# Kernel tuning notes

Measured on AMD Instinct MI355X. Metric: run time of the kernel, lower is better.

Reference implementation:

```python
import jax, jax.numpy as jnp
import numpy as np

DIM = 2
WIDTH = 128
N = 262144
T = 101
W0 = 44.0


def setup_inputs() -> dict:
    key = jax.random.key(0)
    ks = jax.random.split(key, 7)
    # time grid: arange scaled to [0, 1] (dt = 0.01)
    t = jnp.arange(T, dtype=jnp.float32) / (T - 1)
    x0 = jax.random.normal(ks[0], (N, DIM), dtype=jnp.float32)
    # SIREN init: first layer U(-1/dim, 1/dim); later layers U(-sqrt(6/fan_in)/w0, +)
    c0 = 1.0 / DIM
    ch = float(np.sqrt(6.0 / WIDTH) / W0)
    W1 = jax.random.uniform(ks[1], (DIM, WIDTH), jnp.float32, -c0, c0)
    b1 = jax.random.uniform(ks[2], (WIDTH,), jnp.float32, -c0, c0)
    W2 = jax.random.uniform(ks[3], (WIDTH, WIDTH), jnp.float32, -ch, ch)
    b2 = jax.random.uniform(ks[4], (WIDTH,), jnp.float32, -ch, ch)
    W3 = jax.random.uniform(ks[5], (WIDTH, DIM), jnp.float32, -ch, ch)
    b3 = jax.random.uniform(ks[6], (DIM,), jnp.float32, -ch, ch)
    return {"t": t, "x0": x0, "W1": W1, "b1": b1, "W2": W2, "b2": b2, "W3": W3, "b3": b3}


def reference(t, x0, W1, b1, W2, b2, W3, b3):
    def f(x):
        h = jnp.sin(W0 * (x @ W1 + b1))   # [N, WIDTH]
        h = jnp.sin(W0 * (h @ W2 + b2))   # [N, WIDTH]
        return h @ W3 + b3                # [N, DIM]

    # torchdiffeq fixed-grid 'rk4' uses the 3/8-rule (rk4_alt_step_func)
    def step(y, dt):
        k1 = f(y)
        k2 = f(y + dt * k1 / 3.0)
        k3 = f(y + dt * (k2 - k1 / 3.0))
        k4 = f(y + dt * (k1 - k2 + k3))
        y1 = y + (k1 + 3.0 * (k2 + k3) + k4) * dt * 0.125
        return y1, y1

    dts = t[1:] - t[:-1]                  # [T-1]
    _, ys = jax.lax.scan(step, x0, dts)   # [T-1, N, DIM]
    return jnp.concatenate([x0[None], ys], axis=0)  # [T, N, DIM]
```

## Files before the change

kernel.cpp:

```cpp
#include <hip/hip_runtime.h>


#define W0F    44.0f
#define INV2PI 0.15915494309189535f
#define SCALE  (W0F * INV2PI)
#define WIDTH  128
#define NPART  262144
#define TSTEPS 101

typedef short s16x8 __attribute__((ext_vector_type(8)));
typedef float f32x4 __attribute__((ext_vector_type(4)));

__device__ __forceinline__ float sin_rev(float z) {
    return __builtin_amdgcn_sinf(__builtin_amdgcn_fractf(z));
}
__device__ __forceinline__ unsigned short f2bf(float x) {
    __bf16 b = (__bf16)x;
    return __builtin_bit_cast(unsigned short, b);
}
__device__ __forceinline__ float bf2f(unsigned short u) {
    unsigned int v = ((unsigned int)u) << 16;
    return __builtin_bit_cast(float, v);
}

#define ROR_ADD(x, ctrl) ((x) + __builtin_bit_cast(float, \
    __builtin_amdgcn_update_dpp(0, __builtin_bit_cast(int, (x)), (ctrl), 0xF, 0xF, false)))
__device__ __forceinline__ float row_sum16(float x) {
    x = ROR_ADD(x, 0x128);
    x = ROR_ADD(x, 0x124);
    x = ROR_ADD(x, 0x122);
    x = ROR_ADD(x, 0x121);
    return x;
}

__device__ __forceinline__ float sel16(const float g[16], int idx) {
    float a[8], b[4], c[2];
    #pragma unroll
    for (int i = 0; i < 8; ++i) a[i] = (idx & 8) ? g[i + 8] : g[i];
    #pragma unroll
    for (int i = 0; i < 4; ++i) b[i] = (idx & 4) ? a[i + 4] : a[i];
    #pragma unroll
    for (int i = 0; i < 2; ++i) c[i] = (idx & 2) ? b[i + 2] : b[i];
    return (idx & 1) ? c[1] : c[0];
}

__global__ void prep_kernel(const float* __restrict__ W1, const float* __restrict__ b1,
                            const float* __restrict__ W2, float* __restrict__ ws) {
    int i = blockIdx.x * blockDim.x + threadIdx.x;
    unsigned short* whi = (unsigned short*)ws;
    unsigned short* wlo = whi + 16384;
    if (i < 16384) {
        int j = i & 7, l = (i >> 3) & 63, c = (i >> 9) & 3, nt = (i >> 11) & 7;
        int k = 32 * c + 8 * (l >> 4) + j;
        int n = 16 * nt + (l & 15);
        float v = SCALE * W2[k * WIDTH + n];
        unsigned short hi = f2bf(v);
        whi[i] = hi;
        wlo[i] = f2bf(v - bf2f(hi));
    }
    if (i < 2 * WIDTH) ws[16384 + i] = SCALE * W1[i];
    if (i < WIDTH)     ws[16384 + 256 + i] = SCALE * b1[i];
}

__launch_bounds__(256, 2)
__global__ void ode_kernel(const float* __restrict__ t,
                           const float2* __restrict__ x0,
                           const float* __restrict__ ws,
                           const float* __restrict__ W3,
                           const float* __restrict__ b2,
                           const float* __restrict__ b3,
                           float2* __restrict__ out) {
    __shared__ unsigned int sBh[8192];
    __shared__ unsigned int sBl[8192];
    __shared__ __align__(16) float sWx[WIDTH], sWy[WIDTH], sWb[WIDTH];
    __shared__ float2 sW3[WIDTH];
    __shared__ float  sB2[WIDTH];

    const int tid = threadIdx.x;
    const int wave = tid >> 6;
    const int lane = tid & 63;
    const int lane15 = lane & 15;
    const int kg = lane >> 4;

    {
        const uint4* srch = (const uint4*)ws;
        const uint4* srcl = (const uint4*)(ws + 8192);
        uint4* dsth = (uint4*)sBh;
        uint4* dstl = (uint4*)sBl;
        #pragma unroll
        for (int j = 0; j < 8; ++j) {
            dsth[tid + 256 * j] = srch[tid + 256 * j];
            dstl[tid + 256 * j] = srcl[tid + 256 * j];
        }
    }
    if (tid < WIDTH) {
        sWx[tid] = ws[16384 + tid];
        sWy[tid] = ws[16384 + WIDTH + tid];
        sWb[tid] = ws[16384 + 256 + tid];
        sW3[tid] = make_float2(W3[2 * tid], W3[2 * tid + 1]);
        sB2[tid] = SCALE * b2[tid];
    }
    __syncthreads();

    const int mloc = 16 * (lane15 >> 2) + 4 * kg + (lane15 & 3);
    const int p = blockIdx.x * 256 + wave * 64 + mloc;

    float2 y = x0[p];
    out[p] = y;

    const float b30 = b3[0], b31 = b3[1];

    float tprev = t[0];
    #pragma unroll 1
    for (int step = 0; step < TSTEPS - 1; ++step) {
        const float tnext = t[step + 1];
        const float dt = tnext - tprev;
        tprev = tnext;

        float k1x=0.f,k1y=0.f,k2x=0.f,k2y=0.f,k3x=0.f,k3y=0.f,sx=0.f,sy=0.f;

        #pragma unroll 1
        for (int s = 0; s < 4; ++s) {
            float yinx, yiny;
            if (s == 0)      { yinx = y.x;                                 yiny = y.y; }
            else if (s == 1) { const float c1 = dt * (1.0f / 3.0f);
                               yinx = y.x + c1 * k1x;                       yiny = y.y + c1 * k1y; }
            else if (s == 2) { yinx = y.x + dt * (k2x - (1.0f/3.0f) * k1x); yiny = y.y + dt * (k2y - (1.0f/3.0f) * k1y); }
            else             { yinx = y.x + dt * (k1x - k2x + k3x);         yiny = y.y + dt * (k1y - k2y + k3y); }

            float qx[4], qy[4];
            {
                const int sbase = 16 * (lane15 >> 2) + (lane15 & 3);
                qx[0] = __shfl(yinx, sbase,      64); qy[0] = __shfl(yiny, sbase,      64);
                qx[1] = __shfl(yinx, sbase + 4,  64); qy[1] = __shfl(yiny, sbase + 4,  64);
                qx[2] = __shfl(yinx, sbase + 8,  64); qy[2] = __shfl(yiny, sbase + 8,  64);
                qx[3] = __shfl(yinx, sbase + 12, 64); qy[3] = __shfl(yiny, sbase + 12, 64);
            }

            f32x4 acc[8][4];
            #pragma unroll
            for (int i = 0; i < 8; ++i) {
                const float bb = sB2[16 * i + lane15];
                const f32x4 v4 = (f32x4){bb, bb, bb, bb};
                #pragma unroll
                for (int mt = 0; mt < 4; ++mt) acc[i][mt] = v4;
            }

            #pragma unroll 1
            for (int c = 0; c < 4; ++c) {
                uint4 ah[4], al[4];
                #pragma unroll
                for (int jq = 0; jq < 2; ++jq) {
                    float4 wxv = *(const float4*)&sWx[32 * c + 8 * kg + 4 * jq];
                    float4 wyv = *(const float4*)&sWy[32 * c + 8 * kg + 4 * jq];
                    float4 wbv = *(const float4*)&sWb[32 * c + 8 * kg + 4 * jq];
                    #pragma unroll
                    for (int mt = 0; mt < 4; ++mt) {
                        float v0 = sin_rev(fmaf(qx[mt], wxv.x, fmaf(qy[mt], wyv.x, wbv.x)));
                        float v1 = sin_rev(fmaf(qx[mt], wxv.y, fmaf(qy[mt], wyv.y, wbv.y)));
                        float v2 = sin_rev(fmaf(qx[mt], wxv.z, fmaf(qy[mt], wyv.z, wbv.z)));
                        float v3 = sin_rev(fmaf(qx[mt], wxv.w, fmaf(qy[mt], wyv.w, wbv.w)));
                        unsigned short h0 = f2bf(v0), h1 = f2bf(v1);
                        unsigned short h2 = f2bf(v2), h3 = f2bf(v3);
                        unsigned int hA = (unsigned int)h0 | ((unsigned int)h1 << 16);
                        unsigned int hB = (unsigned int)h2 | ((unsigned int)h3 << 16);
                        unsigned int lA = (unsigned int)f2bf(v0 - bf2f(h0)) |
                                          ((unsigned int)f2bf(v1 - bf2f(h1)) << 16);
                        unsigned int lB = (unsigned int)f2bf(v2 - bf2f(h2)) |
                                          ((unsigned int)f2bf(v3 - bf2f(h3)) << 16);
                        if (jq == 0) { ah[mt].x = hA; ah[mt].y = hB;
                                       al[mt].x = lA; al[mt].y = lB; }
                        else         { ah[mt].z = hA; ah[mt].w = hB;
                                       al[mt].z = lA; al[mt].w = lB; }
                    }
                }

                #pragma unroll
                for (int nt = 0; nt < 8; ++nt) {
                    const int fo = (nt * 4 + c) * 256 + lane * 4;
                    uint4 bhU = *(const uint4*)&sBh[fo];
                    uint4 blU = *(const uint4*)&sBl[fo];
                    s16x8 bh = __builtin_bit_cast(s16x8, bhU);
                    s16x8 bl = __builtin_bit_cast(s16x8, blU);
                    #pragma unroll
                    for (int mt = 0; mt < 4; ++mt) {
                        s16x8 ahv = __builtin_bit_cast(s16x8, ah[mt]);
                        s16x8 alv = __builtin_bit_cast(s16x8, al[mt]);
                        acc[nt][mt] = __builtin_amdgcn_mfma_f32_16x16x32_bf16(ahv, bh, acc[nt][mt], 0, 0, 0);
                        acc[nt][mt] = __builtin_amdgcn_mfma_f32_16x16x32_bf16(alv, bh, acc[nt][mt], 0, 0, 0);
                        acc[nt][mt] = __builtin_amdgcn_mfma_f32_16x16x32_bf16(ahv, bl, acc[nt][mt], 0, 0, 0);
                    }
                }
            }

            float gx[16], gy[16];
            #pragma unroll
            for (int i = 0; i < 16; ++i) { gx[i] = 0.f; gy[i] = 0.f; }
            #pragma unroll
            for (int nt = 0; nt < 8; ++nt) {
                float2 w3v = sW3[16 * nt + lane15];
                #pragma unroll
                for (int mt = 0; mt < 4; ++mt) {
                    #pragma unroll
                    for (int r = 0; r < 4; ++r) {
                        float sn = sin_rev(acc[nt][mt][r]);
                        gx[4*mt+r] = fmaf(sn, w3v.x, gx[4*mt+r]);
                        gy[4*mt+r] = fmaf(sn, w3v.y, gy[4*mt+r]);
                    }
                }
            }
            #pragma unroll
            for (int i = 0; i < 16; ++i) { gx[i] = row_sum16(gx[i]); gy[i] = row_sum16(gy[i]); }
            const float fx = b30 + sel16(gx, lane15);
            const float fy = b31 + sel16(gy, lane15);

            if (s == 0)      { k1x = fx; k1y = fy; sx = fx;        sy = fy; }
            else if (s == 1) { k2x = fx; k2y = fy; sx += 3.f * fx; sy += 3.f * fy; }
            else if (s == 2) { k3x = fx; k3y = fy; sx += 3.f * fx; sy += 3.f * fy; }
            else             {                     sx += fx;       sy += fy; }
        }

        const float cc = dt * 0.125f;
        y.x += sx * cc;
        y.y += sy * cc;
        out[(size_t)(step + 1) * NPART + p] = y;
    }
}

extern "C" void kernel_launch(void* const* d_in, const int* in_sizes, int n_in,
                              void* d_out, int out_size, void* d_ws, size_t ws_size,
                              hipStream_t stream) {
    const float*  t  = (const float*)d_in[0];
    const float2* x0 = (const float2*)d_in[1];
    const float*  W1 = (const float*)d_in[2];
    const float*  b1 = (const float*)d_in[3];
    const float*  W2 = (const float*)d_in[4];
    const float*  b2 = (const float*)d_in[5];
    const float*  W3 = (const float*)d_in[6];
    const float*  b3 = (const float*)d_in[7];
    float* ws = (float*)d_ws;
    float2* out = (float2*)d_out;

    prep_kernel<<<64, 256, 0, stream>>>(W1, b1, W2, ws);
    ode_kernel<<<NPART / 256, 256, 0, stream>>>(t, x0, ws, W3, b2, b3, out);
}
```

Before: 10.42 ms.

## Software-pipeline layer-1 sin/A-fragment build with MFMA chunks, cheaper bf16 split

The K-chunk loop is fully unrolled with double-buffered A fragments, so the sin evaluation and bf16 packing for the next chunk can overlap with the MFMAs of the current chunk. The hi/lo bf16 split now truncates and packs with v_perm instead of rounding conversions, which cuts VALU work at slightly lower precision in the hi part. The fract range reduction before sin is also dropped, relying on the hardware sin accepting unreduced revolutions. This raises register pressure under the 2-blocks launch bound and may lose accuracy for large arguments.

```diff
diff --git a/kernel.cpp b/kernel.cpp
--- a/kernel.cpp
+++ b/kernel.cpp
@@ -12,7 +12,7 @@
 typedef float f32x4 __attribute__((ext_vector_type(4)));
 
 __device__ __forceinline__ float sin_rev(float z) {
-    return __builtin_amdgcn_sinf(__builtin_amdgcn_fractf(z));
+    return __builtin_amdgcn_sinf(z);
 }
 __device__ __forceinline__ unsigned short f2bf(float x) {
     __bf16 b = (__bf16)x;
@@ -21,6 +21,14 @@
 __device__ __forceinline__ float bf2f(unsigned short u) {
     unsigned int v = ((unsigned int)u) << 16;
     return __builtin_bit_cast(float, v);
+}
+__device__ __forceinline__ float trunc16f(float v) {
+    return __builtin_bit_cast(float, __builtin_bit_cast(unsigned int, v) & 0xffff0000u);
+}
+__device__ __forceinline__ unsigned int pack_hi16(float vlo, float vhi) {
+    return __builtin_amdgcn_perm(__builtin_bit_cast(unsigned int, vhi),
+                                 __builtin_bit_cast(unsigned int, vlo),
+                                 0x07060302u);
 }
 
 #define ROR_ADD(x, ctrl) ((x) + __builtin_bit_cast(float, \
@@ -62,6 +70,34 @@
     if (i < WIDTH)     ws[16384 + 256 + i] = SCALE * b1[i];
 }
 
+#define BUILD_A(cc, AH, AL)                                                          \
+    {                                                                                \
+        _Pragma("unroll")                                                            \
+        for (int jq = 0; jq < 2; ++jq) {                                             \
+            float4 wxv = *(const float4*)&sWx[32 * (cc) + 8 * kg + 4 * jq];          \
+            float4 wyv = *(const float4*)&sWy[32 * (cc) + 8 * kg + 4 * jq];          \
+            float4 wbv = *(const float4*)&sWb[32 * (cc) + 8 * kg + 4 * jq];          \
+            _Pragma("unroll")                                                        \
+            for (int mt = 0; mt < 4; ++mt) {                                         \
+                float v0 = sin_rev(fmaf(qx[mt], wxv.x, fmaf(qy[mt], wyv.x, wbv.x))); \
+                float v1 = sin_rev(fmaf(qx[mt], wxv.y, fmaf(qy[mt], wyv.y, wbv.y))); \
+                float v2 = sin_rev(fmaf(qx[mt], wxv.z, fmaf(qy[mt], wyv.z, wbv.z))); \
+                float v3 = sin_rev(fmaf(qx[mt], wxv.w, fmaf(qy[mt], wyv.w, wbv.w))); \
+                float r0 = v0 - trunc16f(v0);                                        \
+                float r1 = v1 - trunc16f(v1);                                        \
+                float r2 = v2 - trunc16f(v2);                                        \
+                float r3 = v3 - trunc16f(v3);                                        \
+                if (jq == 0) {                                                       \
+                    AH[mt].x = pack_hi16(v0, v1); AH[mt].y = pack_hi16(v2, v3);      \
+                    AL[mt].x = pack_hi16(r0, r1); AL[mt].y = pack_hi16(r2, r3);      \
+                } else {                                                             \
+                    AH[mt].z = pack_hi16(v0, v1); AH[mt].w = pack_hi16(v2, v3);      \
+                    AL[mt].z = pack_hi16(r0, r1); AL[mt].w = pack_hi16(r2, r3);      \
+                }                                                                    \
+            }                                                                        \
+        }                                                                            \
+    }
+
 __launch_bounds__(256, 2)
 __global__ void ode_kernel(const float* __restrict__ t,
                            const float2* __restrict__ x0,
@@ -146,34 +182,11 @@
                 for (int mt = 0; mt < 4; ++mt) acc[i][mt] = v4;
             }
 
-            #pragma unroll 1
+            uint4 ah[2][4], al[2][4];
+            BUILD_A(0, ah[0], al[0])
+            #pragma unroll
             for (int c = 0; c < 4; ++c) {
-                uint4 ah[4], al[4];
-                #pragma unroll
-                for (int jq = 0; jq < 2; ++jq) {
-                    float4 wxv = *(const float4*)&sWx[32 * c + 8 * kg + 4 * jq];
-                    float4 wyv = *(const float4*)&sWy[32 * c + 8 * kg + 4 * jq];
-                    float4 wbv = *(const float4*)&sWb[32 * c + 8 * kg + 4 * jq];
-                    #pragma unroll
-                    for (int mt = 0; mt < 4; ++mt) {
-                        float v0 = sin_rev(fmaf(qx[mt], wxv.x, fmaf(qy[mt], wyv.x, wbv.x)));
-                        float v1 = sin_rev(fmaf(qx[mt], wxv.y, fmaf(qy[mt], wyv.y, wbv.y)));
-                        float v2 = sin_rev(fmaf(qx[mt], wxv.z, fmaf(qy[mt], wyv.z, wbv.z)));
-                        float v3 = sin_rev(fmaf(qx[mt], wxv.w, fmaf(qy[mt], wyv.w, wbv.w)));
-                        unsigned short h0 = f2bf(v0), h1 = f2bf(v1);
-                        unsigned short h2 = f2bf(v2), h3 = f2bf(v3);
-                        unsigned int hA = (unsigned int)h0 | ((unsigned int)h1 << 16);
-                        unsigned int hB = (unsigned int)h2 | ((unsigned int)h3 << 16);
-                        unsigned int lA = (unsigned int)f2bf(v0 - bf2f(h0)) |
-                                          ((unsigned int)f2bf(v1 - bf2f(h1)) << 16);
-                        unsigned int lB = (unsigned int)f2bf(v2 - bf2f(h2)) |
-                                          ((unsigned int)f2bf(v3 - bf2f(h3)) << 16);
-                        if (jq == 0) { ah[mt].x = hA; ah[mt].y = hB;
-                                       al[mt].x = lA; al[mt].y = lB; }
-                        else         { ah[mt].z = hA; ah[mt].w = hB;
-                                       al[mt].z = lA; al[mt].w = lB; }
-                    }
-                }
+                if (c < 3) BUILD_A(c + 1, ah[(c + 1) & 1], al[(c + 1) & 1])
 
                 #pragma unroll
                 for (int nt = 0; nt < 8; ++nt) {
@@ -184,8 +197,8 @@
                     s16x8 bl = __builtin_bit_cast(s16x8, blU);
                     #pragma unroll
                     for (int mt = 0; mt < 4; ++mt) {
-                        s16x8 ahv = __builtin_bit_cast(s16x8, ah[mt]);
-                        s16x8 alv = __builtin_bit_cast(s16x8, al[mt]);
+                        s16x8 ahv = __builtin_bit_cast(s16x8, ah[c & 1][mt]);
+                        s16x8 alv = __builtin_bit_cast(s16x8, al[c & 1][mt]);
                         acc[nt][mt] = __builtin_amdgcn_mfma_f32_16x16x32_bf16(ahv, bh, acc[nt][mt], 0, 0, 0);
                         acc[nt][mt] = __builtin_amdgcn_mfma_f32_16x16x32_bf16(alv, bh, acc[nt][mt], 0, 0, 0);
                         acc[nt][mt] = __builtin_amdgcn_mfma_f32_16x16x32_bf16(ahv, bl, acc[nt][mt], 0, 0, 0);
```

Result: slower. 30.84 ms (+195.8%).
